# Kernel tuning notes

Measured on AMD Instinct MI355X. Metric: run time of the kernel, lower is better.

Reference implementation:

```python
import jax, jax.numpy as jnp
import numpy as np

VX, VY = 0.16, 0.16
X_OFFSET = VX / 2 + 0.0      # vx/2 + offset[0]
Y_OFFSET = VY / 2 + (-39.68) # vy/2 + offset[1]
BN_EPS = 1e-5
V, P, C_IN, C_OUT = 40000, 32, 4, 64


def setup_inputs() -> dict:
    key = jax.random.key(0)
    k0, k1, k2, k3 = jax.random.split(key, 4)
    voxels = jax.random.normal(k0, (V, P, C_IN), dtype=jnp.float32)
    num_point_per_voxel = jnp.maximum(
        jax.random.randint(k1, (V,), 0, P + 1), 1).astype(jnp.int32)
    coors = jax.random.randint(k2, (V, 2), 0, 400).astype(jnp.int32)
    W = jax.random.normal(k3, (C_OUT, C_IN + 5), dtype=jnp.float32) * 0.1
    gamma = jnp.ones((C_OUT,), dtype=jnp.float32)
    beta = jnp.zeros((C_OUT,), dtype=jnp.float32)
    return {"voxels": voxels, "num_point_per_voxel": num_point_per_voxel,
            "coors": coors, "W": W, "gamma": gamma, "beta": beta}


def reference(voxels, num_point_per_voxel, coors, W, gamma, beta):
    npts = num_point_per_voxel.astype(voxels.dtype)  # [V]
    xyz = voxels[:, :, :3]
    # cluster offset: subtract per-pillar mean of valid points
    points_mean = jnp.sum(xyz, axis=1, keepdims=True) / npts[:, None, None]
    f_cluster = xyz - points_mean  # [V, P, 3]
    # pillar-center offset
    cx = coors[:, 0].astype(voxels.dtype) * VX + X_OFFSET  # [V]
    cy = coors[:, 1].astype(voxels.dtype) * VY + Y_OFFSET
    f_center = jnp.stack([voxels[:, :, 0] - cx[:, None],
                          voxels[:, :, 1] - cy[:, None]], axis=-1)  # [V, P, 2]
    features = jnp.concatenate([voxels, f_cluster, f_center], axis=-1)  # [V, P, 9]
    # zero out padded points
    point_ids = jnp.arange(P, dtype=jnp.int32)[None, :]
    mask = (num_point_per_voxel[:, None] > point_ids).astype(features.dtype)
    features = features * mask[:, :, None]
    # 1x1 conv == per-point linear: [V, P, 9] x [64, 9] -> [V, P, 64]
    x = jnp.einsum('vpc,oc->vpo', features, W)
    # BatchNorm1d (train mode): stats over (voxel, point) dims per channel
    mean = jnp.mean(x, axis=(0, 1))
    var = jnp.var(x, axis=(0, 1))
    x = (x - mean) * jax.lax.rsqrt(var + BN_EPS) * gamma + beta
    x = jax.nn.relu(x)
    # max over points -> [V, 64]
    return jnp.max(x, axis=1)
```

## Files before the change

kernel.cpp:

```cpp
#include <hip/hip_runtime.h>
#include <hip/hip_bf16.h>

#define V_N   40000
#define P_N   32
#define NTOT  (V_N * P_N)
#define VXc   0.16f
#define VYc   0.16f
#define XOFF  0.08f
#define YOFF  (-39.6f)
#define BN_EPS 1e-5f

#define SBLK  250
#define PBLK  2500
#define CSTR  32

#define FOR_S(X) X(0) X(1) X(2) X(3) X(4) X(5) X(6) X(7) X(8)
#define FOR_M(X) \
  X(0,0) X(0,1) X(0,2) X(0,3) X(0,4) X(0,5) X(0,6) X(0,7) X(0,8) \
  X(1,1) X(1,2) X(1,3) X(1,4) X(1,5) X(1,6) X(1,7) X(1,8) \
  X(2,2) X(2,3) X(2,4) X(2,5) X(2,6) X(2,7) X(2,8) \
  X(3,3) X(3,4) X(3,5) X(3,6) X(3,7) X(3,8) \
  X(4,4) X(4,5) X(4,6) X(4,7) X(4,8) \
  X(5,5) X(5,6) X(5,7) X(5,8) \
  X(6,6) X(6,7) X(6,8) \
  X(7,7) X(7,8) \
  X(8,8)

__device__ __forceinline__ float wave_sum(float x) {
#pragma unroll
    for (int m = 1; m < 64; m <<= 1) x += __shfl_xor(x, m, 64);
    return x;
}

__device__ __forceinline__ float rdlane(float x, int l) {
    return __uint_as_float(__builtin_amdgcn_readlane(__float_as_uint(x), l));
}

__global__ __launch_bounds__(256) void stats_kernel(
    const float4* __restrict__ voxels,
    const int*    __restrict__ npts_arr,
    const int*    __restrict__ coors,
    float*        __restrict__ stats,
    float4*       __restrict__ means)
{
    const int lane = threadIdx.x & 63;
    const int p    = lane & 31;
    const int half = lane >> 5;
    const int gw   = (blockIdx.x * 256 + threadIdx.x) >> 6;
    const int nw   = (SBLK * 256) >> 6;

#define DECL_S(i)   float S##i = 0.f;
#define DECL_M(i,j) float M##i##_##j = 0.f;
    FOR_S(DECL_S)
    FOR_M(DECL_M)

    for (int vb = gw * 2; vb < V_N; vb += nw * 2) {
        const int v = vb + half;
        float4 q = voxels[(size_t)v * P_N + p];

        float sx = q.x, sy = q.y, sz = q.z;
#pragma unroll
        for (int m = 1; m < 32; m <<= 1) {
            sx += __shfl_xor(sx, m, 64);
            sy += __shfl_xor(sy, m, 64);
            sz += __shfl_xor(sz, m, 64);
        }
        const int   npts = npts_arr[v];
        const float inv  = 1.f / (float)npts;
        const float mx = sx * inv, my = sy * inv, mz = sz * inv;
        const float cx = (float)coors[2 * v]     * VXc + XOFF;
        const float cy = (float)coors[2 * v + 1] * VYc + YOFF;

        if (p == 0) means[v] = make_float4(mx, my, mz, 0.f);

        const float g  = (p < npts) ? 1.f : 0.f;
        const float f0 = q.x * g;
        const float f1 = q.y * g;
        const float f2 = q.z * g;
        const float f3 = q.w * g;
        const float f4 = (q.x - mx) * g;
        const float f5 = (q.y - my) * g;
        const float f6 = (q.z - mz) * g;
        const float f7 = (q.x - cx) * g;
        const float f8 = (q.y - cy) * g;

#define ACC_S(i)   S##i += f##i;
#define ACC_M(i,j) M##i##_##j = fmaf(f##i, f##j, M##i##_##j);
        FOR_S(ACC_S)
        FOR_M(ACC_M)
    }

#define RED_S(i)   S##i = wave_sum(S##i);
#define RED_M(i,j) M##i##_##j = wave_sum(M##i##_##j);
    FOR_S(RED_S)
    FOR_M(RED_M)

    __shared__ float red[4][54];
    const int wib = threadIdx.x >> 6;
    if (lane == 0) {
        float* r = red[wib];
        int k = 0;
#define ST_S(i)   r[k++] = S##i;
#define ST_M(i,j) r[k++] = M##i##_##j;
        FOR_S(ST_S)
        FOR_M(ST_M)
    }
    __syncthreads();
    if (threadIdx.x < 54) {
        float s = red[0][threadIdx.x] + red[1][threadIdx.x]
                + red[2][threadIdx.x] + red[3][threadIdx.x];
        atomicAdd(&stats[threadIdx.x * CSTR], s);
    }
}

__global__ __launch_bounds__(256) void pfn_kernel(
    const float4* __restrict__ voxels,
    const int*    __restrict__ npts_arr,
    const int*    __restrict__ coors,
    const float*  __restrict__ W,
    const float*  __restrict__ gamma,
    const float*  __restrict__ beta,
    const float*  __restrict__ stats,
    const float4* __restrict__ means,
    float*        __restrict__ out)
{
    const int lane = threadIdx.x & 63;
    const int wib  = threadIdx.x >> 6;

    float w[9];
#pragma unroll
    for (int c = 0; c < 9; ++c) w[c] = W[lane * 9 + c];

    const float invN = 1.f / (float)NTOT;
    float mean = 0.f;
#pragma unroll
    for (int c = 0; c < 9; ++c) mean = fmaf(w[c], stats[c * CSTR], mean);
    mean *= invN;

    float ex2 = 0.f;
    {
        int k = 9;
#pragma unroll
        for (int i = 0; i < 9; ++i)
#pragma unroll
            for (int j = i; j < 9; ++j) {
                const float coef = (i == j) ? 1.f : 2.f;
                ex2 = fmaf(coef * w[i] * w[j], stats[k * CSTR], ex2);
                ++k;
            }
    }
    ex2 *= invN;
    const float var   = ex2 - mean * mean;
    const float scale = gamma[lane] * rsqrtf(var + BN_EPS);
    const float bias  = fmaf(-mean, scale, beta[lane]);

    const float a0 = (w[0] + w[4] + w[7]) * scale;
    const float a1 = (w[1] + w[5] + w[8]) * scale;
    const float a2 = (w[2] + w[6]) * scale;
    const float a3 =  w[3] * scale;
    const float u4 = w[4] * scale, u5 = w[5] * scale, u6 = w[6] * scale;
    const float u7 = w[7] * scale, u8 = w[8] * scale;

    const int gwave = blockIdx.x * 4 + wib;

#define DOT(P_, OFS_) \
    fmaf(rdlane(q.x, (P_) + (OFS_)), a0, \
    fmaf(rdlane(q.y, (P_) + (OFS_)), a1, \
    fmaf(rdlane(q.z, (P_) + (OFS_)), a2, \
         rdlane(q.w, (P_) + (OFS_)) * a3)))

#pragma unroll
    for (int it = 0; it < 2; ++it) {
        const int vA = gwave * 4 + it * 2;
        const int vB = vA + 1;

        const int vv = vA + (lane >> 5);
        const float4 q = voxels[(size_t)vv * P_N + (lane & 31)];

        const int nA = __builtin_amdgcn_readfirstlane(npts_arr[vA]);
        const int nB = __builtin_amdgcn_readfirstlane(npts_arr[vB]);

        const float4 mA = means[vA];
        const float4 mB = means[vB];
        const float cxA = (float)coors[2 * vA]     * VXc + XOFF;
        const float cyA = (float)coors[2 * vA + 1] * VYc + YOFF;
        const float cxB = (float)coors[2 * vB]     * VXc + XOFF;
        const float cyB = (float)coors[2 * vB + 1] * VYc + YOFF;

        const float bA = -fmaf(mA.x, u4, fmaf(mA.y, u5, fmaf(mA.z, u6,
                           fmaf(cxA, u7, cyA * u8))));
        const float bB = -fmaf(mB.x, u4, fmaf(mB.y, u5, fmaf(mB.z, u6,
                           fmaf(cxB, u7, cyB * u8))));

        float e0 = -3.4e38f, e1 = -3.4e38f;
        {
            int p = 0;
            for (; p + 1 < nA; p += 2) {
                const float d0 = DOT(p, 0);
                const float d1 = DOT(p + 1, 0);
                e0 = fmaxf(e0, d0);
                e1 = fmaxf(e1, d1);
            }
            if (p < nA) e0 = fmaxf(e0, DOT(p, 0));
        }
        float mfA = fmaxf(e0, e1) + bA;
        if (nA < P_N) mfA = fmaxf(mfA, 0.f);
        out[(size_t)vA * 64 + lane] = fmaxf(mfA + bias, 0.f);

        float g0 = -3.4e38f, g1 = -3.4e38f;
        {
            int p = 0;
            for (; p + 1 < nB; p += 2) {
                const float d0 = DOT(p, 32);
                const float d1 = DOT(p + 1, 32);
                g0 = fmaxf(g0, d0);
                g1 = fmaxf(g1, d1);
            }
            if (p < nB) g0 = fmaxf(g0, DOT(p, 32));
        }
        float mfB = fmaxf(g0, g1) + bB;
        if (nB < P_N) mfB = fmaxf(mfB, 0.f);
        out[(size_t)vB * 64 + lane] = fmaxf(mfB + bias, 0.f);
    }
#undef DOT
}

extern "C" void kernel_launch(void* const* d_in, const int* in_sizes, int n_in,
                              void* d_out, int out_size, void* d_ws, size_t ws_size,
                              hipStream_t stream)
{
    const float4* voxels = (const float4*)d_in[0];
    const int*    npts   = (const int*)d_in[1];
    const int*    coors  = (const int*)d_in[2];
    const float*  W      = (const float*)d_in[3];
    const float*  gamma  = (const float*)d_in[4];
    const float*  beta   = (const float*)d_in[5];
    float*        out    = (float*)d_out;

    float*  stats = (float*)d_ws;
    float4* means = (float4*)((char*)d_ws + 8192);

    hipMemsetAsync(stats, 0, 54 * CSTR * sizeof(float), stream);
    stats_kernel<<<SBLK, 256, 0, stream>>>(voxels, npts, coors, stats, means);
    pfn_kernel<<<PBLK, 256, 0, stream>>>(voxels, npts, coors, W, gamma, beta,
                                         stats, means, out);
}
```

Before: 119.2 us.

## Fold BN affine computation into last stats block and grid-stride pfn kernel

The last stats block, found with an atomic ticket, now computes the per-channel scale, bias and folded weights once and writes them to workspace, so each pfn block no longer repeats the 54-term variance computation. The stats block also stores pillar centers next to the means, which removes the coors reads in pfn. The stats loop is unrolled to two loads per iteration for more memory parallelism. The pfn kernel becomes a grid-stride loop with 2048 blocks, and the extra ticket and threadfence add a small serial tail to the stats kernel.

```diff
diff --git a/kernel.cpp b/kernel.cpp
--- a/kernel.cpp
+++ b/kernel.cpp
@@ -11,8 +11,11 @@
 #define BN_EPS 1e-5f
 
 #define SBLK  250
-#define PBLK  2500
+#define PBLK  2048
 #define CSTR  32
+#define TICKET_OFF 6912
+#define AFF_OFF    8192
+#define MEANS_OFF  16384
 
 #define FOR_S(X) X(0) X(1) X(2) X(3) X(4) X(5) X(6) X(7) X(8)
 #define FOR_M(X) \
@@ -40,9 +43,17 @@
     const float4* __restrict__ voxels,
     const int*    __restrict__ npts_arr,
     const int*    __restrict__ coors,
-    float*        __restrict__ stats,
-    float4*       __restrict__ means)
+    const float*  __restrict__ W,
+    const float*  __restrict__ gamma,
+    const float*  __restrict__ beta,
+    float*        __restrict__ ws)
 {
+    float*  stats  = ws;
+    int*    ticket = (int*)((char*)ws + TICKET_OFF);
+    float*  aff    = (float*)((char*)ws + AFF_OFF);
+    float4* means  = (float4*)((char*)ws + MEANS_OFF);
+    float*  cyv    = (float*)((char*)ws + MEANS_OFF + V_N * 16);
+
     const int lane = threadIdx.x & 63;
     const int p    = lane & 31;
     const int half = lane >> 5;
@@ -54,40 +65,45 @@
     FOR_S(DECL_S)
     FOR_M(DECL_M)
 
-    for (int vb = gw * 2; vb < V_N; vb += nw * 2) {
-        const int v = vb + half;
-        float4 q = voxels[(size_t)v * P_N + p];
-
-        float sx = q.x, sy = q.y, sz = q.z;
-#pragma unroll
-        for (int m = 1; m < 32; m <<= 1) {
-            sx += __shfl_xor(sx, m, 64);
-            sy += __shfl_xor(sy, m, 64);
-            sz += __shfl_xor(sz, m, 64);
-        }
-        const int   npts = npts_arr[v];
-        const float inv  = 1.f / (float)npts;
-        const float mx = sx * inv, my = sy * inv, mz = sz * inv;
-        const float cx = (float)coors[2 * v]     * VXc + XOFF;
-        const float cy = (float)coors[2 * v + 1] * VYc + YOFF;
-
-        if (p == 0) means[v] = make_float4(mx, my, mz, 0.f);
-
-        const float g  = (p < npts) ? 1.f : 0.f;
-        const float f0 = q.x * g;
-        const float f1 = q.y * g;
-        const float f2 = q.z * g;
-        const float f3 = q.w * g;
-        const float f4 = (q.x - mx) * g;
-        const float f5 = (q.y - my) * g;
-        const float f6 = (q.z - mz) * g;
-        const float f7 = (q.x - cx) * g;
-        const float f8 = (q.y - cy) * g;
-
 #define ACC_S(i)   S##i += f##i;
 #define ACC_M(i,j) M##i##_##j = fmaf(f##i, f##j, M##i##_##j);
-        FOR_S(ACC_S)
-        FOR_M(ACC_M)
+#define STAT_BODY(q, v)                                                       \
+        {                                                                     \
+            float sx = q.x, sy = q.y, sz = q.z;                               \
+            _Pragma("unroll")                                                 \
+            for (int m = 1; m < 32; m <<= 1) {                                \
+                sx += __shfl_xor(sx, m, 64);                                  \
+                sy += __shfl_xor(sy, m, 64);                                  \
+                sz += __shfl_xor(sz, m, 64);                                  \
+            }                                                                 \
+            const int   npts = npts_arr[v];                                   \
+            const float inv  = 1.f / (float)npts;                             \
+            const float mx = sx * inv, my = sy * inv, mz = sz * inv;          \
+            const float cx = (float)coors[2 * (v)]     * VXc + XOFF;          \
+            const float cy = (float)coors[2 * (v) + 1] * VYc + YOFF;          \
+            if (p == 0) { means[v] = make_float4(mx, my, mz, cx);             \
+                          cyv[v] = cy; }                                      \
+            const float g  = (p < npts) ? 1.f : 0.f;                          \
+            const float f0 = q.x * g;                                         \
+            const float f1 = q.y * g;                                         \
+            const float f2 = q.z * g;                                         \
+            const float f3 = q.w * g;                                         \
+            const float f4 = (q.x - mx) * g;                                  \
+            const float f5 = (q.y - my) * g;                                  \
+            const float f6 = (q.z - mz) * g;                                  \
+            const float f7 = (q.x - cx) * g;                                  \
+            const float f8 = (q.y - cy) * g;                                  \
+            FOR_S(ACC_S)                                                      \
+            FOR_M(ACC_M)                                                      \
+        }
+
+    for (int vb = gw * 4; vb < V_N; vb += nw * 4) {
+        const int vA = vb + half;
+        const int vB = vb + 2 + half;
+        float4 q1 = voxels[(size_t)vA * P_N + p];
+        float4 q2 = voxels[(size_t)vB * P_N + p];
+        STAT_BODY(q1, vA)
+        STAT_BODY(q2, vB)
     }
 
 #define RED_S(i)   S##i = wave_sum(S##i);
@@ -111,55 +127,80 @@
                 + red[2][threadIdx.x] + red[3][threadIdx.x];
         atomicAdd(&stats[threadIdx.x * CSTR], s);
     }
+
+    __threadfence();
+    __shared__ int lastflag;
+    if (threadIdx.x == 0)
+        lastflag = (atomicAdd(ticket, 1) == SBLK - 1) ? 1 : 0;
+    __syncthreads();
+    if (lastflag && threadIdx.x < 64) {
+        const int o = threadIdx.x;
+        float st[54];
+#pragma unroll
+        for (int i = 0; i < 54; ++i)
+            st[i] = atomicAdd(&stats[i * CSTR], 0.f);
+
+        float w[9];
+#pragma unroll
+        for (int c = 0; c < 9; ++c) w[c] = W[o * 9 + c];
+
+        const float invN = 1.f / (float)NTOT;
+        float mean = 0.f;
+#pragma unroll
+        for (int c = 0; c < 9; ++c) mean = fmaf(w[c], st[c], mean);
+        mean *= invN;
+
+        float ex2 = 0.f;
+        int k = 9;
+#pragma unroll
+        for (int i = 0; i < 9; ++i)
+#pragma unroll
+            for (int j = i; j < 9; ++j) {
+                const float coef = (i == j) ? 1.f : 2.f;
+                ex2 = fmaf(coef * w[i] * w[j], st[k], ex2);
+                ++k;
+            }
+        ex2 *= invN;
+        const float var   = ex2 - mean * mean;
+        const float scale = gamma[o] * rsqrtf(var + BN_EPS);
+        const float bias  = fmaf(-mean, scale, beta[o]);
+
+        aff[0 * 64 + o] = (w[0] + w[4] + w[7]) * scale;
+        aff[1 * 64 + o] = (w[1] + w[5] + w[8]) * scale;
+        aff[2 * 64 + o] = (w[2] + w[6]) * scale;
+        aff[3 * 64 + o] =  w[3] * scale;
+        aff[4 * 64 + o] =  w[4] * scale;
+        aff[5 * 64 + o] =  w[5] * scale;
+        aff[6 * 64 + o] =  w[6] * scale;
+        aff[7 * 64 + o] =  w[7] * scale;
+        aff[8 * 64 + o] =  w[8] * scale;
+        aff[9 * 64 + o] =  bias;
+    }
 }
 
 __global__ __launch_bounds__(256) void pfn_kernel(
     const float4* __restrict__ voxels,
     const int*    __restrict__ npts_arr,
-    const int*    __restrict__ coors,
-    const float*  __restrict__ W,
-    const float*  __restrict__ gamma,
-    const float*  __restrict__ beta,
-    const float*  __restrict__ stats,
-    const float4* __restrict__ means,
+    const float*  __restrict__ ws,
     float*        __restrict__ out)
 {
+    const float*  aff   = (const float*)((const char*)ws + AFF_OFF);
+    const float4* means = (const float4*)((const char*)ws + MEANS_OFF);
+    const float*  cyv   = (const float*)((const char*)ws + MEANS_OFF + V_N * 16);
+
     const int lane = threadIdx.x & 63;
     const int wib  = threadIdx.x >> 6;
 
-    float w[9];
-#pragma unroll
-    for (int c = 0; c < 9; ++c) w[c] = W[lane * 9 + c];
-
-    const float invN = 1.f / (float)NTOT;
-    float mean = 0.f;
-#pragma unroll
-    for (int c = 0; c < 9; ++c) mean = fmaf(w[c], stats[c * CSTR], mean);
-    mean *= invN;
-
-    float ex2 = 0.f;
-    {
-        int k = 9;
-#pragma unroll
-        for (int i = 0; i < 9; ++i)
-#pragma unroll
-            for (int j = i; j < 9; ++j) {
-                const float coef = (i == j) ? 1.f : 2.f;
-                ex2 = fmaf(coef * w[i] * w[j], stats[k * CSTR], ex2);
-                ++k;
-            }
-    }
-    ex2 *= invN;
-    const float var   = ex2 - mean * mean;
-    const float scale = gamma[lane] * rsqrtf(var + BN_EPS);
-    const float bias  = fmaf(-mean, scale, beta[lane]);
-
-    const float a0 = (w[0] + w[4] + w[7]) * scale;
-    const float a1 = (w[1] + w[5] + w[8]) * scale;
-    const float a2 = (w[2] + w[6]) * scale;
-    const float a3 =  w[3] * scale;
-    const float u4 = w[4] * scale, u5 = w[5] * scale, u6 = w[6] * scale;
-    const float u7 = w[7] * scale, u8 = w[8] * scale;
+    const float a0   = aff[0 * 64 + lane];
+    const float a1   = aff[1 * 64 + lane];
+    const float a2   = aff[2 * 64 + lane];
+    const float a3   = aff[3 * 64 + lane];
+    const float u4   = aff[4 * 64 + lane];
+    const float u5   = aff[5 * 64 + lane];
+    const float u6   = aff[6 * 64 + lane];
+    const float u7   = aff[7 * 64 + lane];
+    const float u8   = aff[8 * 64 + lane];
+    const float bias = aff[9 * 64 + lane];
 
     const int gwave = blockIdx.x * 4 + wib;
 
@@ -169,9 +210,8 @@
     fmaf(rdlane(q.z, (P_) + (OFS_)), a2, \
          rdlane(q.w, (P_) + (OFS_)) * a3)))
 
-#pragma unroll
-    for (int it = 0; it < 2; ++it) {
-        const int vA = gwave * 4 + it * 2;
+    for (int pr = gwave; pr < V_N / 2; pr += PBLK * 4) {
+        const int vA = pr * 2;
         const int vB = vA + 1;
 
         const int vv = vA + (lane >> 5);
@@ -182,15 +222,13 @@
 
         const float4 mA = means[vA];
         const float4 mB = means[vB];
-        const float cxA = (float)coors[2 * vA]     * VXc + XOFF;
-        const float cyA = (float)coors[2 * vA + 1] * VYc + YOFF;
-        const float cxB = (float)coors[2 * vB]     * VXc + XOFF;
-        const float cyB = (float)coors[2 * vB + 1] * VYc + YOFF;
+        const float cyA = cyv[vA];
+        const float cyB = cyv[vB];
 
         const float bA = -fmaf(mA.x, u4, fmaf(mA.y, u5, fmaf(mA.z, u6,
-                           fmaf(cxA, u7, cyA * u8))));
+                           fmaf(mA.w, u7, cyA * u8))));
         const float bB = -fmaf(mB.x, u4, fmaf(mB.y, u5, fmaf(mB.z, u6,
-                           fmaf(cxB, u7, cyB * u8))));
+                           fmaf(mB.w, u7, cyB * u8))));
 
         float e0 = -3.4e38f, e1 = -3.4e38f;
         {
@@ -236,12 +274,9 @@
     const float*  gamma  = (const float*)d_in[4];
     const float*  beta   = (const float*)d_in[5];
     float*        out    = (float*)d_out;
-
-    float*  stats = (float*)d_ws;
-    float4* means = (float4*)((char*)d_ws + 8192);
-
-    hipMemsetAsync(stats, 0, 54 * CSTR * sizeof(float), stream);
-    stats_kernel<<<SBLK, 256, 0, stream>>>(voxels, npts, coors, stats, means);
-    pfn_kernel<<<PBLK, 256, 0, stream>>>(voxels, npts, coors, W, gamma, beta,
-                                         stats, means, out);
-}
+    float*        ws     = (float*)d_ws;
+
+    hipMemsetAsync(d_ws, 0, 8192, stream);
+    stats_kernel<<<SBLK, 256, 0, stream>>>(voxels, npts, coors, W, gamma, beta, ws);
+    pfn_kernel<<<PBLK, 256, 0, stream>>>(voxels, npts, ws, out);
+}
```

Result: slower. 141.9 us (+19.0%).
